# Optimization experiments

Measured on AMD Instinct MI355X. Metric: run time of the kernel, lower is better.

Reference implementation:

```python
import jax, jax.numpy as jnp
import numpy as np

NUM_USERS = 100000
NUM_ITEMS = 50000
LATENT_DIM = 64
N_EDGES = 600000
BATCH = 4096
N_LAYERS = 4  # K=4, time_split=4, euler -> 4 unit propagation steps


def setup_inputs() -> dict:
    key = jax.random.key(0)
    k1, k2, k3, k4, k5, k6 = jax.random.split(key, 6)
    return {
        "users": jax.random.randint(k1, (BATCH,), 0, NUM_USERS),
        "items": jax.random.randint(k2, (BATCH,), 0, NUM_ITEMS),
        "edge_u": jax.random.randint(k3, (N_EDGES,), 0, NUM_USERS),
        "edge_i": jax.random.randint(k4, (N_EDGES,), 0, NUM_ITEMS),
        "user_emb": 0.1 * jax.random.normal(k5, (NUM_USERS, LATENT_DIM), dtype=jnp.float32),
        "item_emb": 0.1 * jax.random.normal(k6, (NUM_ITEMS, LATENT_DIM), dtype=jnp.float32),
    }


def reference(users, items, edge_u, edge_i, user_emb, item_emb):
    num_users = user_emb.shape[0]
    num_items = item_emb.shape[0]
    N = num_users + num_items

    # symmetric bipartite adjacency as directed edge list
    src = jnp.concatenate([edge_u, edge_i + num_users])
    dst = jnp.concatenate([edge_i + num_users, edge_u])

    # D^{-1/2} A D^{-1/2} edge weights (LightGCN normalization)
    deg = jax.ops.segment_sum(jnp.ones_like(src, dtype=jnp.float32), src, num_segments=N)
    inv_sqrt = jnp.where(deg > 0, jax.lax.rsqrt(jnp.maximum(deg, 1.0)), 0.0)
    w = inv_sqrt[src] * inv_sqrt[dst]  # [2E]

    def spmm(x):  # A_hat @ x via gather-scale-scatter
        return jax.ops.segment_sum(w[:, None] * x[src], dst, num_segments=N)

    x0 = jnp.concatenate([user_emb, item_emb], axis=0)  # [N, d]
    # ODE euler step x + A x, then residual subtraction -> stored emb = A^k x0
    embs = [x0]
    e = x0
    for _ in range(N_LAYERS):
        e = spmm(e)
        embs.append(e)
    light_out = jnp.mean(jnp.stack(embs, axis=1), axis=1)  # [N, d]

    all_users = light_out[:num_users]
    all_items = light_out[num_users:]
    users_emb = all_users[users]
    items_emb = all_items[items]
    gamma = jnp.sum(users_emb * items_emb, axis=1)  # [B]
    return gamma
```

## Files before the change

kernel.cpp:

```cpp
#include <hip/hip_runtime.h>

#define WAVE 64
#define BROWS 256
#define NBKT_MAX 1024
#define CMAX 4
#define SRCMASK 0x3FFFF
#define EPB 2048
#define ENTCAP 4096


__device__ __forceinline__ unsigned short f2bf(float f) {
    unsigned u = __float_as_uint(f);
    u += 0x7FFF + ((u >> 16) & 1);
    return (unsigned short)(u >> 16);
}
__device__ __forceinline__ float bf2f(unsigned short v) {
    return __uint_as_float((unsigned)v << 16);
}
__device__ __forceinline__ void addbf8(float* a, uint4 v) {
    a[0] += __uint_as_float(v.x << 16);
    a[1] += __uint_as_float(v.x & 0xFFFF0000u);
    a[2] += __uint_as_float(v.y << 16);
    a[3] += __uint_as_float(v.y & 0xFFFF0000u);
    a[4] += __uint_as_float(v.z << 16);
    a[5] += __uint_as_float(v.z & 0xFFFF0000u);
    a[6] += __uint_as_float(v.w << 16);
    a[7] += __uint_as_float(v.w & 0xFFFF0000u);
}

__global__ void k_hist(const int* __restrict__ eu, const int* __restrict__ ei,
                       int nE, int nU, int nBkt, int nJg, int* __restrict__ cntBB) {
    __shared__ int h4[4 * NBKT_MAX];
    for (int i = threadIdx.x; i < 4 * nBkt; i += 256) h4[i] = 0;
    __syncthreads();
    int* hw = h4 + (threadIdx.x >> 6) * nBkt;
    const int4* eu4 = (const int4*)eu;
    const int4* ei4 = (const int4*)ei;
    for (int pass = 0; pass < 2; pass++) {
        int i4 = blockIdx.x * 512 + pass * 256 + threadIdx.x;
        int e0 = i4 * 4;
        if (e0 + 3 < nE) {
            int4 u = eu4[i4];
            int4 v = ei4[i4];
            atomicAdd(&hw[u.x >> 8], 1); atomicAdd(&hw[(nU + v.x) >> 8], 1);
            atomicAdd(&hw[u.y >> 8], 1); atomicAdd(&hw[(nU + v.y) >> 8], 1);
            atomicAdd(&hw[u.z >> 8], 1); atomicAdd(&hw[(nU + v.z) >> 8], 1);
            atomicAdd(&hw[u.w >> 8], 1); atomicAdd(&hw[(nU + v.w) >> 8], 1);
        } else if (e0 < nE) {
            for (int e = e0; e < nE; e++) {
                atomicAdd(&hw[eu[e] >> 8], 1);
                atomicAdd(&hw[(nU + ei[e]) >> 8], 1);
            }
        }
    }
    __syncthreads();
    int j = (blockIdx.x & 7) * nJg + (blockIdx.x >> 3);
    int* dst = cntBB + (size_t)j * nBkt;
    for (int i = threadIdx.x; i < nBkt; i += 256)
        dst[i] = h4[i] + h4[nBkt + i] + h4[2 * nBkt + i] + h4[3 * nBkt + i];
}

__global__ void k_scanBkt(const int* __restrict__ cntBB, int* __restrict__ baseBB,
                          int* __restrict__ bktTot, int nBkt, int nJ) {
    __shared__ int s[256];
    int b = blockIdx.x, t = threadIdx.x;
    int C = (nJ + 255) / 256;
    int vals[CMAX];
    int sum = 0;
    for (int k = 0; k < CMAX; k++) {
        if (k >= C) break;
        int j = t * C + k;
        int v = (j < nJ) ? cntBB[(size_t)j * nBkt + b] : 0;
        vals[k] = v; sum += v;
    }
    s[t] = sum;
    __syncthreads();
    for (int o = 1; o < 256; o <<= 1) {
        int x = (t >= o) ? s[t - o] : 0;
        __syncthreads();
        s[t] += x;
        __syncthreads();
    }
    int run = s[t] - sum;
    for (int k = 0; k < CMAX; k++) {
        if (k >= C) break;
        int j = t * C + k;
        if (j < nJ) { baseBB[(size_t)b * nJ + j] = run; run += vals[k]; }
    }
    if (t == 0) bktTot[b] = s[255];
}

__global__ void k_scanTot(const int* __restrict__ bktTot, int* __restrict__ bktBase,
                          int* __restrict__ row_ptr, int nBkt, int N, int total) {
    __shared__ int s[1024];
    int t = threadIdx.x;
    int v = (t < nBkt) ? bktTot[t] : 0;
    s[t] = v;
    __syncthreads();
    for (int o = 1; o < 1024; o <<= 1) {
        int x = (t >= o) ? s[t - o] : 0;
        __syncthreads();
        s[t] += x;
        __syncthreads();
    }
    if (t < nBkt) bktBase[t] = s[t] - v;
    if (t == 0) { bktBase[nBkt] = total; row_ptr[N] = total; }
}

__global__ void k_bin(const int* __restrict__ eu, const int* __restrict__ ei,
                      int nE, int nU, int nBkt, int nJ, int nJg,
                      const int* __restrict__ baseBB, const int* __restrict__ bktBase,
                      int* __restrict__ bins) {
    __shared__ int cur[NBKT_MAX];
    int j = (blockIdx.x & 7) * nJg + (blockIdx.x >> 3);
    for (int i = threadIdx.x; i < nBkt; i += 256)
        cur[i] = bktBase[i] + baseBB[(size_t)i * nJ + j];
    __syncthreads();
    const int4* eu4 = (const int4*)eu;
    const int4* ei4 = (const int4*)ei;
    for (int pass = 0; pass < 2; pass++) {
        int i4 = blockIdx.x * 512 + pass * 256 + threadIdx.x;
        int e0 = i4 * 4;
        if (e0 + 3 < nE) {
            int4 uu = eu4[i4];
            int4 vv = ei4[i4];
            #pragma unroll
            for (int k = 0; k < 4; k++) {
                int u = (k == 0) ? uu.x : (k == 1) ? uu.y : (k == 2) ? uu.z : uu.w;
                int i2 = (k == 0) ? vv.x : (k == 1) ? vv.y : (k == 2) ? vv.z : vv.w;
                int v = nU + i2;
                int p1 = atomicAdd(&cur[u >> 8], 1);
                int p2 = atomicAdd(&cur[v >> 8], 1);
                bins[p1] = ((u & 255) << 18) | v;
                bins[p2] = ((v & 255) << 18) | u;
            }
        } else if (e0 < nE) {
            for (int e = e0; e < nE; e++) {
                int u = eu[e];
                int v = nU + ei[e];
                int p1 = atomicAdd(&cur[u >> 8], 1);
                int p2 = atomicAdd(&cur[v >> 8], 1);
                bins[p1] = ((u & 255) << 18) | v;
                bins[p2] = ((v & 255) << 18) | u;
            }
        }
    }
}

__global__ void k_csrz(const int* __restrict__ bins, const int* __restrict__ bktBase,
                       int N, int nU,
                       const float* __restrict__ ue, const float* __restrict__ ie,
                       int* __restrict__ row_ptr, int* __restrict__ col,
                       unsigned short* __restrict__ z0) {
    __shared__ int ent[ENTCAP];
    __shared__ int h4[4 * BROWS];
    __shared__ int sc[BROWS];
    __shared__ int cur4[4 * BROWS];
    __shared__ float sInv[BROWS];
    int b = blockIdx.x, t = threadIdx.x, w = t >> 6;
    int base = bktBase[b];
    int n = bktBase[b + 1] - base;
    h4[t] = 0; h4[256 + t] = 0; h4[512 + t] = 0; h4[768 + t] = 0;
    __syncthreads();
    int* hw = h4 + w * BROWS;
    for (int i = t; i < n; i += 256) {
        int p = bins[base + i];
        if (i < ENTCAP) ent[i] = p;
        atomicAdd(&hw[p >> 18], 1);
    }
    __syncthreads();
    int v = h4[t] + h4[256 + t] + h4[512 + t] + h4[768 + t];
    sc[t] = v;
    __syncthreads();
    for (int o = 1; o < 256; o <<= 1) {
        int x = (t >= o) ? sc[t - o] : 0;
        __syncthreads();
        sc[t] += x;
        __syncthreads();
    }
    int excl = sc[t] - v;
    int row = b * BROWS + t;
    if (row < N) row_ptr[row] = base + excl;
    sInv[t] = (v > 0) ? (1.0f / sqrtf((float)v)) : 0.0f;
    cur4[t]       = excl;
    cur4[256 + t] = excl + h4[t];
    cur4[512 + t] = excl + h4[t] + h4[256 + t];
    cur4[768 + t] = excl + h4[t] + h4[256 + t] + h4[512 + t];
    __syncthreads();
    int rf = t & 15, rg = t >> 4;
    for (int pass = 0; pass < 16; pass++) {
        int r = pass * 16 + rg;
        int rr = b * BROWS + r;
        if (rr < N) {
            const float4* src = (rr < nU)
                ? ((const float4*)ue) + (size_t)rr * 16
                : ((const float4*)ie) + (size_t)(rr - nU) * 16;
            float4 val = src[rf];
            float scl = sInv[r];
            ushort4 o;
            o.x = f2bf(val.x * scl);
            o.y = f2bf(val.y * scl);
            o.z = f2bf(val.z * scl);
            o.w = f2bf(val.w * scl);
            ((ushort4*)z0)[(size_t)rr * 16 + rf] = o;
        }
    }
    int* cw = cur4 + w * BROWS;
    for (int i = t; i < n; i += 256) {
        int p = (i < ENTCAP) ? ent[i] : bins[base + i];
        int pos = base + atomicAdd(&cw[p >> 18], 1);
        col[pos] = p & SRCMASK;
    }
}

__global__ void k_spmm(const int* __restrict__ row_ptr, const int* __restrict__ col,
                       const unsigned short* __restrict__ x,
                       unsigned short* __restrict__ y, int N, int nBlkMain,
                       const int* __restrict__ users, const int* __restrict__ items,
                       int B, int nU,
                       const float* __restrict__ ue, const float* __restrict__ ie,
                       float* __restrict__ acc, int mode) {
    int t = threadIdx.x;
    if ((int)blockIdx.x < nBlkMain) {
        int grp = t >> 3, f = t & 7;
        int row = blockIdx.x * 32 + grp;
        if (row >= N) return;
        const uint4* x8 = (const uint4*)x;
        int s = row_ptr[row], e = row_ptr[row + 1];
        float a0[8] = {0,0,0,0,0,0,0,0};
        float a1[8] = {0,0,0,0,0,0,0,0};
        float a2[8] = {0,0,0,0,0,0,0,0};
        float a3[8] = {0,0,0,0,0,0,0,0};
        int j = s;
        for (; j + 3 < e; j += 4) {
            int c0 = col[j], c1 = col[j + 1], c2 = col[j + 2], c3 = col[j + 3];
            uint4 v0 = x8[(size_t)c0 * 8 + f];
            uint4 v1 = x8[(size_t)c1 * 8 + f];
            uint4 v2 = x8[(size_t)c2 * 8 + f];
            uint4 v3 = x8[(size_t)c3 * 8 + f];
            addbf8(a0, v0); addbf8(a1, v1); addbf8(a2, v2); addbf8(a3, v3);
        }
        for (; j < e; j++) {
            uint4 v = x8[(size_t)col[j] * 8 + f];
            addbf8(a0, v);
        }
        float rdeg = (e > s) ? (1.0f / (float)(e - s)) : 0.0f;
        uint4 o;
        float s0, s1;
        s0 = (a0[0]+a1[0]+a2[0]+a3[0]) * rdeg; s1 = (a0[1]+a1[1]+a2[1]+a3[1]) * rdeg;
        o.x = (unsigned)f2bf(s0) | ((unsigned)f2bf(s1) << 16);
        s0 = (a0[2]+a1[2]+a2[2]+a3[2]) * rdeg; s1 = (a0[3]+a1[3]+a2[3]+a3[3]) * rdeg;
        o.y = (unsigned)f2bf(s0) | ((unsigned)f2bf(s1) << 16);
        s0 = (a0[4]+a1[4]+a2[4]+a3[4]) * rdeg; s1 = (a0[5]+a1[5]+a2[5]+a3[5]) * rdeg;
        o.z = (unsigned)f2bf(s0) | ((unsigned)f2bf(s1) << 16);
        s0 = (a0[6]+a1[6]+a2[6]+a3[6]) * rdeg; s1 = (a0[7]+a1[7]+a2[7]+a3[7]) * rdeg;
        o.w = (unsigned)f2bf(s0) | ((unsigned)f2bf(s1) << 16);
        ((uint4*)y)[(size_t)row * 8 + f] = o;
    } else {
        int grp = t >> 4, f4 = t & 15;
        int b = (blockIdx.x - nBlkMain) * 16 + grp;
        if (b >= 2 * B) return;
        const ushort4* x4 = (const ushort4*)x;
        float4 c;
        if (mode == 0) {
            const float4* x0 = (b < B)
                ? ((const float4*)ue) + (size_t)users[b] * 16
                : ((const float4*)ie) + (size_t)items[b - B] * 16;
            c = x0[f4];
        } else {
            int row = (b < B) ? users[b] : (nU + items[b - B]);
            int deg = row_ptr[row + 1] - row_ptr[row];
            float f = sqrtf((float)deg);
            ushort4 v = x4[(size_t)row * 16 + f4];
            c = ((const float4*)acc)[(size_t)b * 16 + f4];
            c.x += f * bf2f(v.x); c.y += f * bf2f(v.y);
            c.z += f * bf2f(v.z); c.w += f * bf2f(v.w);
        }
        ((float4*)acc)[(size_t)b * 16 + f4] = c;
    }
}

__global__ void k_tail34(const int* __restrict__ row_ptr, const int* __restrict__ col,
                         const unsigned short* __restrict__ z3,
                         const int* __restrict__ users, const int* __restrict__ items,
                         int B, int nU, float* __restrict__ acc) {
    int t = threadIdx.x, grp = t >> 3, f = t & 7;
    int b = blockIdx.x * 32 + grp;
    if (b >= 2 * B) return;
    int row = (b < B) ? users[b] : (nU + items[b - B]);
    int s = row_ptr[row], e = row_ptr[row + 1];
    const uint4* x8 = (const uint4*)z3;
    float4 cA = ((const float4*)acc)[(size_t)b * 16 + 2 * f];
    float4 cB = ((const float4*)acc)[(size_t)b * 16 + 2 * f + 1];
    if (e > s) {
        float fq = sqrtf((float)(e - s));
        float a0[8] = {0,0,0,0,0,0,0,0};
        float a1[8] = {0,0,0,0,0,0,0,0};
        int j = s;
        for (; j + 1 < e; j += 2) {
            uint4 v0 = x8[(size_t)col[j] * 8 + f];
            uint4 v1 = x8[(size_t)col[j + 1] * 8 + f];
            addbf8(a0, v0); addbf8(a1, v1);
        }
        if (j < e) {
            uint4 v0 = x8[(size_t)col[j] * 8 + f];
            addbf8(a0, v0);
        }
        uint4 vs = x8[(size_t)row * 8 + f];
        float self[8] = {0,0,0,0,0,0,0,0};
        addbf8(self, vs);
        float scale = fq / (float)(e - s);
        cA.x += fq * self[0] + scale * (a0[0] + a1[0]);
        cA.y += fq * self[1] + scale * (a0[1] + a1[1]);
        cA.z += fq * self[2] + scale * (a0[2] + a1[2]);
        cA.w += fq * self[3] + scale * (a0[3] + a1[3]);
        cB.x += fq * self[4] + scale * (a0[4] + a1[4]);
        cB.y += fq * self[5] + scale * (a0[5] + a1[5]);
        cB.z += fq * self[6] + scale * (a0[6] + a1[6]);
        cB.w += fq * self[7] + scale * (a0[7] + a1[7]);
    }
    ((float4*)acc)[(size_t)b * 16 + 2 * f]     = cA;
    ((float4*)acc)[(size_t)b * 16 + 2 * f + 1] = cB;
}

__global__ void k_dot(const float* __restrict__ acc, int B, float* __restrict__ out) {
    int b = blockIdx.x * (blockDim.x >> 6) + (threadIdx.x >> 6);
    int lane = threadIdx.x & 63;
    if (b >= B) return;
    float p = acc[(size_t)b * 64 + lane] * acc[(size_t)(b + B) * 64 + lane];
    #pragma unroll
    for (int o = 32; o > 0; o >>= 1) p += __shfl_down(p, o, WAVE);
    if (lane == 0) out[b] = p * (1.0f / 25.0f);
}

extern "C" void kernel_launch(void* const* d_in, const int* in_sizes, int n_in,
                              void* d_out, int out_size, void* d_ws, size_t ws_size,
                              hipStream_t stream) {
    const int*   users = (const int*)d_in[0];
    const int*   items = (const int*)d_in[1];
    const int*   eu    = (const int*)d_in[2];
    const int*   ei    = (const int*)d_in[3];
    const float* ue    = (const float*)d_in[4];
    const float* ie    = (const float*)d_in[5];
    float* out = (float*)d_out;

    const int D  = 64;
    const int B  = in_sizes[0];
    const int nE = in_sizes[2];
    const int nU = in_sizes[4] / D;
    const int nI = in_sizes[5] / D;
    const int N  = nU + nI;
    const int nBkt = (N + BROWS - 1) / BROWS;
    const int total = 2 * nE;

    const int nBlkB = (nE + EPB - 1) / EPB;
    const int nJg   = (nBlkB + 7) / 8;
    const int nJ    = 8 * nJg;

    char* p = (char*)d_ws;
    auto alloc = [&](size_t bytes) -> void* {
        void* r = (void*)p;
        p += (bytes + 255) & ~(size_t)255;
        return r;
    };
    int*   cntBB   = (int*)  alloc((size_t)nJ * nBkt * 4);
    int*   baseBB  = (int*)  alloc((size_t)nBkt * nJ * 4);
    int*   bktTot  = (int*)  alloc((size_t)nBkt * 4);
    int*   bktBase = (int*)  alloc((size_t)(nBkt + 1) * 4);
    int*   bins    = (int*)  alloc((size_t)total * 4);
    int*   col     = (int*)  alloc((size_t)total * 4);
    int*   row_ptr = (int*)  alloc((size_t)(N + 1) * 4);
    unsigned short* za = (unsigned short*)alloc((size_t)N * D * 2);
    unsigned short* zb = (unsigned short*)alloc((size_t)N * D * 2);
    float* acc     = (float*)alloc((size_t)2 * B * D * 4);

    k_hist<<<nJ, 256, 0, stream>>>(eu, ei, nE, nU, nBkt, nJg, cntBB);
    k_scanBkt<<<nBkt, 256, 0, stream>>>(cntBB, baseBB, bktTot, nBkt, nJ);
    k_scanTot<<<1, 1024, 0, stream>>>(bktTot, bktBase, row_ptr, nBkt, N, total);
    k_bin<<<nJ, 256, 0, stream>>>(eu, ei, nE, nU, nBkt, nJ, nJg, baseBB, bktBase, bins);
    k_csrz<<<nBkt, BROWS, 0, stream>>>(bins, bktBase, N, nU, ue, ie, row_ptr, col, za);

    const int nBlkMain = (N + 31) / 32;
    const int nBlkTail = (2 * B + 15) / 16;
    unsigned short* zin = za;
    unsigned short* zout = zb;
    for (int l = 0; l < 3; l++) {
        k_spmm<<<nBlkMain + nBlkTail, 256, 0, stream>>>(
            row_ptr, col, zin, zout, N, nBlkMain,
            users, items, B, nU, ue, ie, acc, (l == 0) ? 0 : 1);
        unsigned short* t = zin; zin = zout; zout = t;
    }

    const int nBlkT34 = (2 * B + 31) / 32;
    k_tail34<<<nBlkT34, 256, 0, stream>>>(row_ptr, col, zin, users, items, B, nU, acc);
    k_dot<<<(B + 3) / 4, 256, 0, stream>>>(acc, B, out);
}
```

Baseline: 220.2 us.

## Skip third-layer SpMM rows not needed by batch and fuse tail with dot

Adds a marking pass that flags the batch users and items plus their direct neighbours. The third propagation step then computes only flagged rows, because only those are read by the final layer's tail. Fuses the tail accumulation with the dot-product kernel, removing one launch and the acc round trip. This costs an extra small kernel, a byte-flag array cleared during CSR build, and a per-row flag check.

```diff
diff --git a/kernel.cpp b/kernel.cpp
--- a/kernel.cpp
+++ b/kernel.cpp
@@ -151,7 +151,8 @@
                        int N, int nU,
                        const float* __restrict__ ue, const float* __restrict__ ie,
                        int* __restrict__ row_ptr, int* __restrict__ col,
-                       unsigned short* __restrict__ z0) {
+                       unsigned short* __restrict__ z0,
+                       unsigned char* __restrict__ flag) {
     __shared__ int ent[ENTCAP];
     __shared__ int h4[4 * BROWS];
     __shared__ int sc[BROWS];
@@ -161,6 +162,10 @@
     int base = bktBase[b];
     int n = bktBase[b + 1] - base;
     h4[t] = 0; h4[256 + t] = 0; h4[512 + t] = 0; h4[768 + t] = 0;
+    {
+        int row = b * BROWS + t;
+        if (row < N) flag[row] = 0;
+    }
     __syncthreads();
     int* hw = h4 + w * BROWS;
     for (int i = t; i < n; i += 256) {
@@ -213,18 +218,31 @@
     }
 }
 
+__global__ void k_mark(const int* __restrict__ row_ptr, const int* __restrict__ col,
+                       const int* __restrict__ users, const int* __restrict__ items,
+                       int B, int nU, unsigned char* __restrict__ flag) {
+    int bi = blockIdx.x * 256 + threadIdx.x;
+    if (bi >= 2 * B) return;
+    int row = (bi < B) ? users[bi] : (nU + items[bi - B]);
+    flag[row] = 1;
+    int s = row_ptr[row], e = row_ptr[row + 1];
+    for (int j = s; j < e; j++) flag[col[j]] = 1;
+}
+
 __global__ void k_spmm(const int* __restrict__ row_ptr, const int* __restrict__ col,
                        const unsigned short* __restrict__ x,
                        unsigned short* __restrict__ y, int N, int nBlkMain,
                        const int* __restrict__ users, const int* __restrict__ items,
                        int B, int nU,
                        const float* __restrict__ ue, const float* __restrict__ ie,
-                       float* __restrict__ acc, int mode) {
+                       float* __restrict__ acc, int mode,
+                       const unsigned char* __restrict__ flag, int doSkip) {
     int t = threadIdx.x;
     if ((int)blockIdx.x < nBlkMain) {
         int grp = t >> 3, f = t & 7;
         int row = blockIdx.x * 32 + grp;
         if (row >= N) return;
+        if (doSkip && !flag[row]) return;
         const uint4* x8 = (const uint4*)x;
         int s = row_ptr[row], e = row_ptr[row + 1];
         float a0[8] = {0,0,0,0,0,0,0,0};
@@ -280,57 +298,55 @@
     }
 }
 
-__global__ void k_tail34(const int* __restrict__ row_ptr, const int* __restrict__ col,
-                         const unsigned short* __restrict__ z3,
-                         const int* __restrict__ users, const int* __restrict__ items,
-                         int B, int nU, float* __restrict__ acc) {
+__global__ void k_dot34(const int* __restrict__ row_ptr, const int* __restrict__ col,
+                        const unsigned short* __restrict__ z3,
+                        const int* __restrict__ users, const int* __restrict__ items,
+                        const float* __restrict__ acc, int B, int nU,
+                        float* __restrict__ out) {
     int t = threadIdx.x, grp = t >> 3, f = t & 7;
     int b = blockIdx.x * 32 + grp;
-    if (b >= 2 * B) return;
-    int row = (b < B) ? users[b] : (nU + items[b - B]);
-    int s = row_ptr[row], e = row_ptr[row + 1];
+    if (b >= B) return;
     const uint4* x8 = (const uint4*)z3;
-    float4 cA = ((const float4*)acc)[(size_t)b * 16 + 2 * f];
-    float4 cB = ((const float4*)acc)[(size_t)b * 16 + 2 * f + 1];
-    if (e > s) {
-        float fq = sqrtf((float)(e - s));
-        float a0[8] = {0,0,0,0,0,0,0,0};
-        float a1[8] = {0,0,0,0,0,0,0,0};
-        int j = s;
-        for (; j + 1 < e; j += 2) {
-            uint4 v0 = x8[(size_t)col[j] * 8 + f];
-            uint4 v1 = x8[(size_t)col[j + 1] * 8 + f];
-            addbf8(a0, v0); addbf8(a1, v1);
-        }
-        if (j < e) {
-            uint4 v0 = x8[(size_t)col[j] * 8 + f];
-            addbf8(a0, v0);
-        }
-        uint4 vs = x8[(size_t)row * 8 + f];
-        float self[8] = {0,0,0,0,0,0,0,0};
-        addbf8(self, vs);
-        float scale = fq / (float)(e - s);
-        cA.x += fq * self[0] + scale * (a0[0] + a1[0]);
-        cA.y += fq * self[1] + scale * (a0[1] + a1[1]);
-        cA.z += fq * self[2] + scale * (a0[2] + a1[2]);
-        cA.w += fq * self[3] + scale * (a0[3] + a1[3]);
-        cB.x += fq * self[4] + scale * (a0[4] + a1[4]);
-        cB.y += fq * self[5] + scale * (a0[5] + a1[5]);
-        cB.z += fq * self[6] + scale * (a0[6] + a1[6]);
-        cB.w += fq * self[7] + scale * (a0[7] + a1[7]);
-    }
-    ((float4*)acc)[(size_t)b * 16 + 2 * f]     = cA;
-    ((float4*)acc)[(size_t)b * 16 + 2 * f + 1] = cB;
-}
-
-__global__ void k_dot(const float* __restrict__ acc, int B, float* __restrict__ out) {
-    int b = blockIdx.x * (blockDim.x >> 6) + (threadIdx.x >> 6);
-    int lane = threadIdx.x & 63;
-    if (b >= B) return;
-    float p = acc[(size_t)b * 64 + lane] * acc[(size_t)(b + B) * 64 + lane];
+    float au[8], ai[8];
     #pragma unroll
-    for (int o = 32; o > 0; o >>= 1) p += __shfl_down(p, o, WAVE);
-    if (lane == 0) out[b] = p * (1.0f / 25.0f);
+    for (int side = 0; side < 2; side++) {
+        float* a = side ? ai : au;
+        int bb = side ? (b + B) : b;
+        int row = side ? (nU + items[b]) : users[b];
+        float4 cA = ((const float4*)acc)[(size_t)bb * 16 + 2 * f];
+        float4 cB = ((const float4*)acc)[(size_t)bb * 16 + 2 * f + 1];
+        a[0] = cA.x; a[1] = cA.y; a[2] = cA.z; a[3] = cA.w;
+        a[4] = cB.x; a[5] = cB.y; a[6] = cB.z; a[7] = cB.w;
+        int s = row_ptr[row], e = row_ptr[row + 1];
+        if (e > s) {
+            float fq = sqrtf((float)(e - s));
+            float g0[8] = {0,0,0,0,0,0,0,0};
+            float g1[8] = {0,0,0,0,0,0,0,0};
+            int j = s;
+            for (; j + 1 < e; j += 2) {
+                uint4 v0 = x8[(size_t)col[j] * 8 + f];
+                uint4 v1 = x8[(size_t)col[j + 1] * 8 + f];
+                addbf8(g0, v0); addbf8(g1, v1);
+            }
+            if (j < e) {
+                uint4 v0 = x8[(size_t)col[j] * 8 + f];
+                addbf8(g0, v0);
+            }
+            float self[8] = {0,0,0,0,0,0,0,0};
+            addbf8(self, x8[(size_t)row * 8 + f]);
+            float scale = fq / (float)(e - s);
+            #pragma unroll
+            for (int k = 0; k < 8; k++)
+                a[k] += fq * self[k] + scale * (g0[k] + g1[k]);
+        }
+    }
+    float p = 0.f;
+    #pragma unroll
+    for (int k = 0; k < 8; k++) p += au[k] * ai[k];
+    p += __shfl_xor(p, 1, WAVE);
+    p += __shfl_xor(p, 2, WAVE);
+    p += __shfl_xor(p, 4, WAVE);
+    if (f == 0) out[b] = p * (1.0f / 25.0f);
 }
 
 extern "C" void kernel_launch(void* const* d_in, const int* in_sizes, int n_in,
@@ -373,12 +389,16 @@
     unsigned short* za = (unsigned short*)alloc((size_t)N * D * 2);
     unsigned short* zb = (unsigned short*)alloc((size_t)N * D * 2);
     float* acc     = (float*)alloc((size_t)2 * B * D * 4);
+    unsigned char* flag = (unsigned char*)alloc((size_t)N);
 
     k_hist<<<nJ, 256, 0, stream>>>(eu, ei, nE, nU, nBkt, nJg, cntBB);
     k_scanBkt<<<nBkt, 256, 0, stream>>>(cntBB, baseBB, bktTot, nBkt, nJ);
     k_scanTot<<<1, 1024, 0, stream>>>(bktTot, bktBase, row_ptr, nBkt, N, total);
     k_bin<<<nJ, 256, 0, stream>>>(eu, ei, nE, nU, nBkt, nJ, nJg, baseBB, bktBase, bins);
-    k_csrz<<<nBkt, BROWS, 0, stream>>>(bins, bktBase, N, nU, ue, ie, row_ptr, col, za);
+    k_csrz<<<nBkt, BROWS, 0, stream>>>(bins, bktBase, N, nU, ue, ie,
+                                       row_ptr, col, za, flag);
+    k_mark<<<(2 * B + 255) / 256, 256, 0, stream>>>(row_ptr, col, users, items,
+                                                    B, nU, flag);
 
     const int nBlkMain = (N + 31) / 32;
     const int nBlkTail = (2 * B + 15) / 16;
@@ -387,11 +407,11 @@
     for (int l = 0; l < 3; l++) {
         k_spmm<<<nBlkMain + nBlkTail, 256, 0, stream>>>(
             row_ptr, col, zin, zout, N, nBlkMain,
-            users, items, B, nU, ue, ie, acc, (l == 0) ? 0 : 1);
+            users, items, B, nU, ue, ie, acc, (l == 0) ? 0 : 1,
+            flag, (l == 2) ? 1 : 0);
         unsigned short* t = zin; zin = zout; zout = t;
     }
 
-    const int nBlkT34 = (2 * B + 31) / 32;
-    k_tail34<<<nBlkT34, 256, 0, stream>>>(row_ptr, col, zin, users, items, B, nU, acc);
-    k_dot<<<(B + 3) / 4, 256, 0, stream>>>(acc, B, out);
-}
+    k_dot34<<<(B + 31) / 32, 256, 0, stream>>>(row_ptr, col, zin, users, items,
+                                               acc, B, nU, out);
+}
```

After: 223.5 us. No clear change (+1.5%).
